# Kernel tuning notes

Measured on AMD Instinct MI355X. Metric: run time of the kernel, lower is better.

## Reference

```python
import jax, jax.numpy as jnp
import numpy as np

B, S, D = 4, 2048, 256
H = 8
KD = D  # keras MHA key_dim = input_shape[-1] -> per-head dim equals D
EPS = 1e-5


def layer_norm(x, gamma, beta):
    mu = jnp.mean(x, axis=-1, keepdims=True)
    var = jnp.var(x, axis=-1, keepdims=True)
    return (x - mu) * jax.lax.rsqrt(var + EPS) * gamma + beta


def setup_inputs() -> dict:
    key = jax.random.key(0)
    ks = jax.random.split(key, 12)
    scale = 1.0 / np.sqrt(D)
    inp = {
        "input_query": jax.random.normal(ks[0], (B, S, D), jnp.float32),
        "key": jax.random.normal(ks[1], (B, S, D), jnp.float32),
        "value": jax.random.normal(ks[2], (B, S, D), jnp.float32),
        # LayerNorm params (3 separate norms)
        "gq": jnp.ones((D,), jnp.float32), "bq_ln": jnp.zeros((D,), jnp.float32),
        "gk": jnp.ones((D,), jnp.float32), "bk_ln": jnp.zeros((D,), jnp.float32),
        "gv": jnp.ones((D,), jnp.float32), "bv_ln": jnp.zeros((D,), jnp.float32),
        # MHA projection weights: [D, H, KD] for q/k/v, [H, KD, D] for output
        "Wq": jax.random.normal(ks[3], (D, H, KD), jnp.float32) * scale,
        "bq": jnp.zeros((H, KD), jnp.float32),
        "Wk": jax.random.normal(ks[4], (D, H, KD), jnp.float32) * scale,
        "bk": jnp.zeros((H, KD), jnp.float32),
        "Wv": jax.random.normal(ks[5], (D, H, KD), jnp.float32) * scale,
        "bv": jnp.zeros((H, KD), jnp.float32),
        "Wo": jax.random.normal(ks[6], (H, KD, D), jnp.float32) * scale,
        "bo": jnp.zeros((D,), jnp.float32),
    }
    return inp


def reference(input_query, key, value, gq, bq_ln, gk, bk_ln, gv, bv_ln,
              Wq, bq, Wk, bk, Wv, bv, Wo, bo):
    # pre-LN on each stream
    q_in = layer_norm(input_query, gq, bq_ln)
    k_in = layer_norm(key, gk, bk_ln)
    v_in = layer_norm(value, gv, bv_ln)

    # projections -> [B, S, H, KD]
    q = jnp.einsum('bsd,dhk->bshk', q_in, Wq) + bq
    k = jnp.einsum('bsd,dhk->bshk', k_in, Wk) + bk
    v = jnp.einsum('bsd,dhk->bshk', v_in, Wv) + bv

    # scaled dot-product attention (keras scales query by 1/sqrt(key_dim))
    q = q * (1.0 / np.sqrt(KD)).astype(np.float32)
    scores = jnp.einsum('bqhk,bshk->bhqs', q, k)  # [B, H, Sq, Sk]
    probs = jax.nn.softmax(scores, axis=-1)
    # dropout = 0.0 (inference)
    attn = jnp.einsum('bhqs,bshk->bqhk', probs, v)
    out = jnp.einsum('bqhk,hkd->bqd', attn, Wo) + bo

    return input_query + out
```

## Files before the change

### kernel.cpp

```cpp
#include <hip/hip_runtime.h>

using bf16x8 = __attribute__((ext_vector_type(8))) __bf16;
using f32x4  = __attribute__((ext_vector_type(4))) float;
using f32x16 = __attribute__((ext_vector_type(16))) float;
using uint2v = __attribute__((ext_vector_type(2))) unsigned;
typedef unsigned short u16;
typedef const __attribute__((address_space(1))) void* gas_p;
typedef __attribute__((address_space(3))) void* las_p;

#define LOG2E 1.4426950408889634f

__device__ __forceinline__ u16 f2bf(float f) {
  union { float f; unsigned u; } v; v.f = f;
  unsigned r = v.u + 0x7fffu + ((v.u >> 16) & 1u);
  return (u16)(r >> 16);
}

__device__ __forceinline__ unsigned pkbf(float a, float b) {
  unsigned r;
  asm("v_cvt_pk_bf16_f32 %0, %1, %2" : "=v"(r) : "v"(a), "v"(b));
  return r;
}

__device__ __forceinline__ float exp2v(float x) {
  float r;
  asm("v_exp_f32 %0, %1" : "=v"(r) : "v"(x));
  return r;
}

__device__ __forceinline__ unsigned pk_fp8x4(float a, float b, float c, float d) {
  int w = __builtin_amdgcn_cvt_pk_fp8_f32(a, b, 0, false);
  w = __builtin_amdgcn_cvt_pk_fp8_f32(c, d, w, true);
  return (unsigned)w;
}

__device__ __forceinline__ uint2v swap32(unsigned a, unsigned b) {
  return __builtin_amdgcn_permlane32_swap(a, b, false, false);
}

__device__ __forceinline__ void gload16(const void* g, void* l) {
  __builtin_amdgcn_global_load_lds((gas_p)g, (las_p)l, 16, 0, 0);
}

#define MFMA(a, b, c)   __builtin_amdgcn_mfma_f32_16x16x32_bf16((a), (b), (c), 0, 0, 0)
#define MFMA32(a, b, c) __builtin_amdgcn_mfma_f32_32x32x16_bf16((a), (b), (c), 0, 0, 0)
#define MFMA8(a, b, c)  __builtin_amdgcn_mfma_f32_32x32x16_fp8_fp8((a), (b), (c), 0, 0, 0)

__global__ __launch_bounds__(256) void transpose_conv(
    const float* __restrict__ Wq, const float* __restrict__ Wk,
    const float* __restrict__ Wv, const float* __restrict__ Wo,
    u16* __restrict__ wqt, u16* __restrict__ wkt,
    u16* __restrict__ wvt, u16* __restrict__ wot)
{
  int z = blockIdx.y;
  const float* src = (z == 0) ? Wq : (z == 1) ? Wk : (z == 2) ? Wv : Wo;
  u16* dst = (z == 0) ? wqt : (z == 1) ? wkt : (z == 2) ? wvt : wot;
  int C = (z < 3) ? 2048 : 256;
  int R = (z < 3) ? 256 : 2048;
  int TC = C >> 5;
  int tc = blockIdx.x % TC, tr = blockIdx.x / TC;
  __shared__ float tile[32][33];
  int j = threadIdx.x & 31, i0 = threadIdx.x >> 5;
#pragma unroll
  for (int p = 0; p < 4; p++)
    tile[i0 + p * 8][j] = src[(tr * 32 + i0 + p * 8) * C + tc * 32 + j];
  __syncthreads();
#pragma unroll
  for (int p = 0; p < 4; p++)
    dst[(tc * 32 + i0 + p * 8) * R + tr * 32 + j] = f2bf(tile[j][i0 + p * 8]);
}

__global__ __launch_bounds__(256) void ln3_kernel(
    const float* __restrict__ xq, const float* __restrict__ xk, const float* __restrict__ xv,
    const float* __restrict__ gq, const float* __restrict__ bq,
    const float* __restrict__ gk, const float* __restrict__ bk,
    const float* __restrict__ gv, const float* __restrict__ bv,
    u16* __restrict__ oq, u16* __restrict__ ok, u16* __restrict__ ov)
{
  int z = blockIdx.y;
  const float* x = (z == 0) ? xq : (z == 1) ? xk : xv;
  const float* g = (z == 0) ? gq : (z == 1) ? gk : gv;
  const float* be = (z == 0) ? bq : (z == 1) ? bk : bv;
  u16* o = (z == 0) ? oq : (z == 1) ? ok : ov;
  int w = threadIdx.x >> 6, l = threadIdx.x & 63;
  int row = blockIdx.x * 4 + w;
  float4 x4 = *(const float4*)(x + row * 256 + l * 4);
  float s = x4.x + x4.y + x4.z + x4.w;
  float sq = x4.x * x4.x + x4.y * x4.y + x4.z * x4.z + x4.w * x4.w;
#pragma unroll
  for (int mm = 1; mm < 64; mm <<= 1) { s += __shfl_xor(s, mm); sq += __shfl_xor(sq, mm); }
  float mu = s * (1.f / 256.f);
  float var = sq * (1.f / 256.f) - mu * mu;
  float rs = rsqrtf(var + 1e-5f);
  float4 g4 = *(const float4*)(g + l * 4);
  float4 b4 = *(const float4*)(be + l * 4);
  ushort4 o4;
  o4.x = f2bf((x4.x - mu) * rs * g4.x + b4.x);
  o4.y = f2bf((x4.y - mu) * rs * g4.y + b4.y);
  o4.z = f2bf((x4.z - mu) * rs * g4.z + b4.z);
  o4.w = f2bf((x4.w - mu) * rs * g4.w + b4.w);
  *(ushort4*)(o + row * 256 + l * 4) = o4;
}

__global__ __launch_bounds__(256) void proj_gemm(
    const u16* __restrict__ qn, const u16* __restrict__ kn, const u16* __restrict__ vn,
    const u16* __restrict__ wqt, const u16* __restrict__ wkt, const u16* __restrict__ wvt,
    const float* __restrict__ bq, const float* __restrict__ bk, const float* __restrict__ bv,
    u16* __restrict__ qo, u16* __restrict__ ko, unsigned char* __restrict__ vo)
{
  __shared__ u16 As[128 * 64];
  __shared__ u16 Bs[128 * 64];
  int z = blockIdx.z;
  const u16* A  = (z == 0) ? qn : (z == 1) ? kn : vn;
  const u16* Bt = (z == 0) ? wqt : (z == 1) ? wkt : wvt;
  const float* bias = (z == 0) ? bq : (z == 1) ? bk : bv;
  float scale = (z == 0) ? 0.0625f * LOG2E : 1.0f;

  int i0 = blockIdx.x * 128, n0 = blockIdx.y * 128;
  int tid = threadIdx.x, w = tid >> 6, l = tid & 63;
  int wr = w >> 1, wc = w & 1, l15 = l & 15, qv = l >> 4;

  f32x4 acc[4][4] = {};

  for (int k0 = 0; k0 < 256; k0 += 64) {
    __syncthreads();
#pragma unroll
    for (int j = 0; j < 4; j++) {
      int c = (w * 4 + j) * 64 + l;
      int row = c >> 3, co = (c & 7) * 8;
      gload16(A + (i0 + row) * 256 + k0 + co, (char*)As + (w * 4 + j) * 1024);
      gload16(Bt + (n0 + row) * 256 + k0 + co, (char*)Bs + (w * 4 + j) * 1024);
    }
    __syncthreads();
#pragma unroll
    for (int kk = 0; kk < 2; kk++) {
      bf16x8 a[4], bfr[4];
#pragma unroll
      for (int m = 0; m < 4; m++)
        a[m] = *(const bf16x8*)(As + (wr * 64 + m * 16 + l15) * 64 + kk * 32 + qv * 8);
#pragma unroll
      for (int n = 0; n < 4; n++)
        bfr[n] = *(const bf16x8*)(Bs + (wc * 64 + n * 16 + l15) * 64 + kk * 32 + qv * 8);
#pragma unroll
      for (int m = 0; m < 4; m++)
#pragma unroll
        for (int n = 0; n < 4; n++) acc[m][n] = MFMA(a[m], bfr[n], acc[m][n]);
    }
  }

  if (z == 2) {
#pragma unroll
    for (int n = 0; n < 4; n++) {
      int col = n0 + wc * 64 + n * 16 + l15;
      float bc = bias[col];
      int hd = col >> 8, kd = col & 255;
#pragma unroll
      for (int m = 0; m < 4; m++) {
        int row0 = i0 + wr * 64 + m * 16 + qv * 4;
        int bb = row0 >> 11, ss = row0 & 2047;
        unsigned wv = pk_fp8x4(acc[m][n][0] + bc, acc[m][n][1] + bc,
                               acc[m][n][2] + bc, acc[m][n][3] + bc);
        int pos = (ss & ~63) | (((ss >> 3) & 3) << 4) | (((ss >> 5) & 1) << 3) | (ss & 7);
        *(unsigned*)(vo + ((size_t)(bb * 8 + hd) * 256 + kd) * 2048 + pos) = wv;
      }
    }
  } else {
    u16* Co = (z == 0) ? qo : ko;
#pragma unroll
    for (int n = 0; n < 4; n++) {
      int col = n0 + wc * 64 + n * 16 + l15;
      float bc = bias[col];
      int hd = col >> 8, kd = col & 255;
#pragma unroll
      for (int m = 0; m < 4; m++) {
#pragma unroll
        for (int r = 0; r < 4; r++) {
          int row = i0 + wr * 64 + m * 16 + qv * 4 + r;
          int bb = row >> 11, ss = row & 2047;
          Co[((bb * 8 + hd) * 2048 + ss) * 256 + kd] = f2bf((acc[m][n][r] + bc) * scale);
        }
      }
    }
  }
}

__global__ __launch_bounds__(512, 2) void flash_attn(
    const u16* __restrict__ q, const u16* __restrict__ k,
    const unsigned char* __restrict__ vt, u16* __restrict__ o)
{
  __shared__ char lds[98304];
  int f = blockIdx.x;
  int qt = f >> 5;
  int bh = (f & 7) | (((f >> 3) & 3) << 3);
  int b = bh >> 3, hh = bh & 7;
  int tid = threadIdx.x, w = tid >> 6, l = tid & 63;
  int l31 = l & 31, h = l >> 5;

  const u16* Q = q + (size_t)(bh * 2048 + qt * 256 + w * 32) * 256;
  const u16* K = k + (size_t)bh * 2048 * 256;
  const unsigned char* V = vt + (size_t)bh * 256 * 2048;

  bf16x8 qf[16];
#pragma unroll
  for (int dt = 0; dt < 16; dt++)
    qf[dt] = *(const bf16x8*)(Q + l31 * 256 + dt * 16 + h * 8);

  f32x16 oacc[8] = {};
  float m_ = -1e30f, lsum = 0.f;

  auto stage = [&](int t, char* base) {
#pragma unroll
    for (int j = 0; j < 4; j++) {
      int c = w * 4 + j;
      int off = c * 1024 + l * 16;
      int r = off >> 9, ps = l & 31;
      gload16(K + (size_t)(t * 64 + r) * 256 + ((ps ^ (r & 31)) << 3), base + off);
    }
#pragma unroll
    for (int j = 0; j < 2; j++) {
      int c = w * 2 + j;
      int off = c * 1024 + l * 16;
      int r = off >> 8, pg = (off >> 4) & 15;
      int g = pg ^ (r & 15);
      int d = r + 64 * (g >> 2), sc = g & 3;
      gload16(V + (size_t)d * 2048 + t * 64 + sc * 16, base + 32768 + off);
    }
  };

  stage(0, lds);
  __syncthreads();

  for (int t = 0; t < 32; t++) {
    char* cur = lds + (size_t)(t & 1) * 49152;
    char* nxt = lds + (size_t)((t + 1) & 1) * 49152;
    if (t + 1 < 32) stage(t + 1, nxt);

    f32x16 p0 = {}, p1 = {};
    __builtin_amdgcn_s_setprio(1);
#pragma unroll
    for (int dt = 0; dt < 16; dt++) {
      int sl = ((dt * 2 + h) ^ l31) << 4;
      bf16x8 kf0 = *(const bf16x8*)(cur + l31 * 512 + sl);
      bf16x8 kf1 = *(const bf16x8*)(cur + (32 + l31) * 512 + sl);
      p0 = MFMA32(kf0, qf[dt], p0);
      p1 = MFMA32(kf1, qf[dt], p1);
    }
    __builtin_amdgcn_s_setprio(0);

    float n0 = fmaxf(fmaxf(p0[0], p0[1]), fmaxf(p0[2], p0[3]));
    float n1 = fmaxf(fmaxf(p0[4], p0[5]), fmaxf(p0[6], p0[7]));
    float n2 = fmaxf(fmaxf(p0[8], p0[9]), fmaxf(p0[10], p0[11]));
    float n3 = fmaxf(fmaxf(p0[12], p0[13]), fmaxf(p0[14], p0[15]));
    float n4 = fmaxf(fmaxf(p1[0], p1[1]), fmaxf(p1[2], p1[3]));
    float n5 = fmaxf(fmaxf(p1[4], p1[5]), fmaxf(p1[6], p1[7]));
    float n6 = fmaxf(fmaxf(p1[8], p1[9]), fmaxf(p1[10], p1[11]));
    float n7 = fmaxf(fmaxf(p1[12], p1[13]), fmaxf(p1[14], p1[15]));
    float mt = fmaxf(fmaxf(fmaxf(n0, n1), fmaxf(n2, n3)),
                     fmaxf(fmaxf(n4, n5), fmaxf(n6, n7)));
    {
      uint2v mr = swap32(__builtin_bit_cast(unsigned, mt), __builtin_bit_cast(unsigned, mt));
      mt = fmaxf(__builtin_bit_cast(float, mr.x), __builtin_bit_cast(float, mr.y));
    }
    if (__any(mt > m_ + 7.0f)) {
      float mn = fmaxf(m_, mt);
      float fsc = exp2v(m_ - mn);
      lsum *= fsc;
#pragma unroll
      for (int dt = 0; dt < 8; dt++)
#pragma unroll
        for (int i = 0; i < 16; i++) oacc[dt][i] *= fsc;
      m_ = mn;
    }
#pragma unroll
    for (int i = 0; i < 16; i++) { p0[i] = exp2v(p0[i] - m_); lsum += p0[i]; }
#pragma unroll
    for (int i = 0; i < 16; i++) { p1[i] = exp2v(p1[i] - m_); lsum += p1[i]; }

    unsigned pwf0[4], pwf1[4];
#pragma unroll
    for (int j = 0; j < 4; j++) {
      pwf0[j] = pk_fp8x4(p0[4 * j], p0[4 * j + 1], p0[4 * j + 2], p0[4 * j + 3]);
      pwf1[j] = pk_fp8x4(p1[4 * j], p1[4 * j + 1], p1[4 * j + 2], p1[4 * j + 3]);
    }

#pragma unroll
    for (int k2 = 0; k2 < 2; k2++) {
      uint2v f0 = swap32(pwf0[k2 * 2], pwf0[k2 * 2 + 1]);
      uint2v f1 = swap32(pwf1[k2 * 2], pwf1[k2 * 2 + 1]);
      long long pA = (long long)(((unsigned long long)f0.y << 32) | f0.x);
      long long pB = (long long)(((unsigned long long)f1.y << 32) | f1.x);
      __builtin_amdgcn_s_setprio(1);
#pragma unroll
      for (int dt = 0; dt < 8; dt++) {
        int r = (dt & 1) * 32 + l31;
        int g = (dt >> 1) * 4 + k2 * 2 + h;
        const uint4 vv = *(const uint4*)(cur + 32768 + r * 256 + ((g ^ (r & 15)) << 4));
        long long vA = (long long)(((unsigned long long)vv.y << 32) | vv.x);
        long long vB = (long long)(((unsigned long long)vv.w << 32) | vv.z);
        oacc[dt] = MFMA8(vA, pA, oacc[dt]);
        oacc[dt] = MFMA8(vB, pB, oacc[dt]);
      }
      __builtin_amdgcn_s_setprio(0);
    }

    asm volatile("s_waitcnt vmcnt(0)" ::: "memory");
    __syncthreads();
  }

  __syncthreads();
  float lsc;
  {
    uint2v lr = swap32(__builtin_bit_cast(unsigned, lsum), __builtin_bit_cast(unsigned, lsum));
    lsc = __builtin_bit_cast(float, lr.x) + __builtin_bit_cast(float, lr.y);
  }
  float inv = 1.0f / lsc;
  char* wbase = (char*)lds + w * 8192;
  int qr15 = l31 & 15;
#pragma unroll
  for (int ph = 0; ph < 2; ph++) {
    if ((l31 >> 4) == ph) {
#pragma unroll
      for (int dt = 0; dt < 8; dt++) {
#pragma unroll
        for (int rg = 0; rg < 4; rg++) {
          uint2 uu;
          uu.x = pkbf(oacc[dt][rg * 4 + 0] * inv, oacc[dt][rg * 4 + 1] * inv);
          uu.y = pkbf(oacc[dt][rg * 4 + 2] * inv, oacc[dt][rg * 4 + 3] * inv);
          *(uint2*)(wbase + qr15 * 512 + ((dt * 64 + rg * 16) ^ (qr15 << 4)) + h * 8) = uu;
        }
      }
    }
    asm volatile("s_waitcnt lgkmcnt(0)" ::: "memory");
    __builtin_amdgcn_sched_barrier(0);
#pragma unroll
    for (int c = 0; c < 8; c++) {
      int qr = c * 2 + h;
      uint4 vv = *(const uint4*)(wbase + qr * 512 + ((l31 ^ qr) << 4));
      int s = qt * 256 + w * 32 + ph * 16 + qr;
      *(uint4*)((char*)o + (size_t)(b * 2048 + s) * 4096 + hh * 512 + l31 * 16) = vv;
    }
    asm volatile("s_waitcnt lgkmcnt(0)" ::: "memory");
  }
}

__global__ __launch_bounds__(256) void out_gemm(
    const u16* __restrict__ A, const u16* __restrict__ Bt,
    const float* __restrict__ bo, const float* __restrict__ resid,
    float* __restrict__ out)
{
  __shared__ u16 As[128 * 64];
  __shared__ u16 Bs[64 * 64];
  int i0 = blockIdx.x * 128, n0 = blockIdx.y * 64;
  int tid = threadIdx.x, w = tid >> 6, l = tid & 63, l15 = l & 15, qv = l >> 4;

  f32x4 acc[2][4] = {};

  for (int k0 = 0; k0 < 2048; k0 += 64) {
    __syncthreads();
#pragma unroll
    for (int j = 0; j < 4; j++) {
      int c = (w * 4 + j) * 64 + l;
      int row = c >> 3, co = (c & 7) * 8;
      gload16(A + (i0 + row) * 2048 + k0 + co, (char*)As + (w * 4 + j) * 1024);
    }
#pragma unroll
    for (int j = 0; j < 2; j++) {
      int c = (w * 2 + j) * 64 + l;
      int row = c >> 3, co = (c & 7) * 8;
      gload16(Bt + (n0 + row) * 2048 + k0 + co, (char*)Bs + (w * 2 + j) * 1024);
    }
    __syncthreads();
#pragma unroll
    for (int kk = 0; kk < 2; kk++) {
      bf16x8 a[2], bfr[4];
#pragma unroll
      for (int m = 0; m < 2; m++)
        a[m] = *(const bf16x8*)(As + (w * 32 + m * 16 + l15) * 64 + kk * 32 + qv * 8);
#pragma unroll
      for (int n = 0; n < 4; n++)
        bfr[n] = *(const bf16x8*)(Bs + (n * 16 + l15) * 64 + kk * 32 + qv * 8);
#pragma unroll
      for (int m = 0; m < 2; m++)
#pragma unroll
        for (int n = 0; n < 4; n++) acc[m][n] = MFMA(a[m], bfr[n], acc[m][n]);
    }
  }

#pragma unroll
  for (int n = 0; n < 4; n++) {
    int col = n0 + n * 16 + l15;
    float bc = bo[col];
#pragma unroll
    for (int m = 0; m < 2; m++)
#pragma unroll
      for (int r = 0; r < 4; r++) {
        int row = i0 + w * 32 + m * 16 + qv * 4 + r;
        out[row * 256 + col] = acc[m][n][r] + bc + resid[row * 256 + col];
      }
  }
}

extern "C" void kernel_launch(void* const* d_in, const int* in_sizes, int n_in,
                              void* d_out, int out_size, void* d_ws, size_t ws_size,
                              hipStream_t stream)
{
  const float* inq  = (const float*)d_in[0];
  const float* key  = (const float*)d_in[1];
  const float* val  = (const float*)d_in[2];
  const float* gq   = (const float*)d_in[3];
  const float* bqln = (const float*)d_in[4];
  const float* gk   = (const float*)d_in[5];
  const float* bkln = (const float*)d_in[6];
  const float* gv   = (const float*)d_in[7];
  const float* bvln = (const float*)d_in[8];
  const float* Wq   = (const float*)d_in[9];
  const float* bq   = (const float*)d_in[10];
  const float* Wk   = (const float*)d_in[11];
  const float* bk   = (const float*)d_in[12];
  const float* Wv   = (const float*)d_in[13];
  const float* bv   = (const float*)d_in[14];
  const float* Wo   = (const float*)d_in[15];
  const float* bo   = (const float*)d_in[16];

  char* ws = (char*)d_ws;
  const size_t MB = 1ull << 20;
  u16* wqt = (u16*)(ws + 0 * MB);
  u16* wkt = (u16*)(ws + 1 * MB);
  u16* wvt = (u16*)(ws + 2 * MB);
  u16* wot = (u16*)(ws + 3 * MB);
  u16* qn  = (u16*)(ws + 4 * MB);
  u16* kn  = (u16*)(ws + 8 * MB);
  u16* vn  = (u16*)(ws + 12 * MB);
  u16* qws = (u16*)(ws + 16 * MB);
  u16* kws = (u16*)(ws + 48 * MB);
  u16* attn = (u16*)(ws + 80 * MB);
  unsigned char* vtw = (unsigned char*)(ws + 112 * MB);

  transpose_conv<<<dim3(512, 4), 256, 0, stream>>>(Wq, Wk, Wv, Wo, wqt, wkt, wvt, wot);
  ln3_kernel<<<dim3(2048, 3), 256, 0, stream>>>(inq, key, val, gq, bqln, gk, bkln, gv, bvln,
                                                qn, kn, vn);
  proj_gemm<<<dim3(64, 16, 3), 256, 0, stream>>>(qn, kn, vn, wqt, wkt, wvt, bq, bk, bv,
                                                 qws, kws, vtw);
  flash_attn<<<256, 512, 0, stream>>>(qws, kws, vtw, attn);
  out_gemm<<<dim3(64, 4), 256, 0, stream>>>(attn, wot, bo, inq, (float*)d_out);
}
```

Measured before the change: 251.5 us.

## Software-pipeline attention loop: defer PV of previous tile behind next QK

Restructures the flash-attention main loop so the P·V MFMAs for tile t-1 are issued right after the QK MFMAs for tile t, overlapping the softmax exp/max work with matrix-core work. K and V staging are split into separate double-buffered LDS regions, with K prefetched two tiles ahead and V one ahead. The per-iteration barrier moves to the end, just before the next loads are issued. The exp-sum reduction is split into four partial accumulators to shorten the dependency chain. This adds register pressure from carrying the packed probabilities between iterations, and the output rescale is now applied after the deferred PV has already accumulated into oacc.

```diff
diff --git a/kernel.cpp b/kernel.cpp
--- a/kernel.cpp
+++ b/kernel.cpp
@@ -207,8 +207,10 @@
 
   f32x16 oacc[8] = {};
   float m_ = -1e30f, lsum = 0.f;
-
-  auto stage = [&](int t, char* base) {
+  unsigned pwp0[4], pwp1[4];
+
+  auto stageK = [&](int t, int slot) {
+    char* base = lds + (size_t)slot * 32768;
 #pragma unroll
     for (int j = 0; j < 4; j++) {
       int c = w * 4 + j;
@@ -216,6 +218,9 @@
       int r = off >> 9, ps = l & 31;
       gload16(K + (size_t)(t * 64 + r) * 256 + ((ps ^ (r & 31)) << 3), base + off);
     }
+  };
+  auto stageV = [&](int t, int slot) {
+    char* base = lds + 65536 + (size_t)slot * 16384;
 #pragma unroll
     for (int j = 0; j < 2; j++) {
       int c = w * 2 + j;
@@ -223,29 +228,51 @@
       int r = off >> 8, pg = (off >> 4) & 15;
       int g = pg ^ (r & 15);
       int d = r + 64 * (g >> 2), sc = g & 3;
-      gload16(V + (size_t)d * 2048 + t * 64 + sc * 16, base + 32768 + off);
+      gload16(V + (size_t)d * 2048 + t * 64 + sc * 16, base + off);
     }
   };
 
-  stage(0, lds);
+  auto pv_prev = [&](const char* vb) {
+#pragma unroll
+    for (int k2 = 0; k2 < 2; k2++) {
+      uint2v f0 = swap32(pwp0[k2 * 2], pwp0[k2 * 2 + 1]);
+      uint2v f1 = swap32(pwp1[k2 * 2], pwp1[k2 * 2 + 1]);
+      long long pA = (long long)(((unsigned long long)f0.y << 32) | f0.x);
+      long long pB = (long long)(((unsigned long long)f1.y << 32) | f1.x);
+      __builtin_amdgcn_s_setprio(1);
+#pragma unroll
+      for (int dt = 0; dt < 8; dt++) {
+        int r = (dt & 1) * 32 + l31;
+        int g = (dt >> 1) * 4 + k2 * 2 + h;
+        const uint4 vv = *(const uint4*)(vb + r * 256 + ((g ^ (r & 15)) << 4));
+        long long vA = (long long)(((unsigned long long)vv.y << 32) | vv.x);
+        long long vB = (long long)(((unsigned long long)vv.w << 32) | vv.z);
+        oacc[dt] = MFMA8(vA, pA, oacc[dt]);
+        oacc[dt] = MFMA8(vB, pB, oacc[dt]);
+      }
+      __builtin_amdgcn_s_setprio(0);
+    }
+  };
+
+  stageK(0, 0); stageK(1, 1); stageV(0, 0);
   __syncthreads();
 
   for (int t = 0; t < 32; t++) {
-    char* cur = lds + (size_t)(t & 1) * 49152;
-    char* nxt = lds + (size_t)((t + 1) & 1) * 49152;
-    if (t + 1 < 32) stage(t + 1, nxt);
+    const char* kb = lds + (size_t)(t & 1) * 32768;
 
     f32x16 p0 = {}, p1 = {};
     __builtin_amdgcn_s_setprio(1);
 #pragma unroll
     for (int dt = 0; dt < 16; dt++) {
       int sl = ((dt * 2 + h) ^ l31) << 4;
-      bf16x8 kf0 = *(const bf16x8*)(cur + l31 * 512 + sl);
-      bf16x8 kf1 = *(const bf16x8*)(cur + (32 + l31) * 512 + sl);
+      bf16x8 kf0 = *(const bf16x8*)(kb + l31 * 512 + sl);
+      bf16x8 kf1 = *(const bf16x8*)(kb + (32 + l31) * 512 + sl);
       p0 = MFMA32(kf0, qf[dt], p0);
       p1 = MFMA32(kf1, qf[dt], p1);
     }
     __builtin_amdgcn_s_setprio(0);
+
+    if (t > 0) pv_prev(lds + 65536 + (size_t)((t - 1) & 1) * 16384);
 
     float n0 = fmaxf(fmaxf(p0[0], p0[1]), fmaxf(p0[2], p0[3]));
     float n1 = fmaxf(fmaxf(p0[4], p0[5]), fmaxf(p0[6], p0[7]));
@@ -261,20 +288,30 @@
       uint2v mr = swap32(__builtin_bit_cast(unsigned, mt), __builtin_bit_cast(unsigned, mt));
       mt = fmaxf(__builtin_bit_cast(float, mr.x), __builtin_bit_cast(float, mr.y));
     }
-    if (__any(mt > m_ + 7.0f)) {
+    bool resc = __any(mt > m_ + 7.0f);
+    float fsc = 1.0f;
+    if (resc) {
       float mn = fmaxf(m_, mt);
-      float fsc = exp2v(m_ - mn);
+      fsc = exp2v(m_ - mn);
       lsum *= fsc;
-#pragma unroll
-      for (int dt = 0; dt < 8; dt++)
-#pragma unroll
-        for (int i = 0; i < 16; i++) oacc[dt][i] *= fsc;
       m_ = mn;
     }
-#pragma unroll
-    for (int i = 0; i < 16; i++) { p0[i] = exp2v(p0[i] - m_); lsum += p0[i]; }
-#pragma unroll
-    for (int i = 0; i < 16; i++) { p1[i] = exp2v(p1[i] - m_); lsum += p1[i]; }
+    float s0 = 0.f, s1 = 0.f, s2 = 0.f, s3 = 0.f;
+#pragma unroll
+    for (int i = 0; i < 16; i += 4) {
+      p0[i] = exp2v(p0[i] - m_);         s0 += p0[i];
+      p0[i + 1] = exp2v(p0[i + 1] - m_); s1 += p0[i + 1];
+      p0[i + 2] = exp2v(p0[i + 2] - m_); s2 += p0[i + 2];
+      p0[i + 3] = exp2v(p0[i + 3] - m_); s3 += p0[i + 3];
+    }
+#pragma unroll
+    for (int i = 0; i < 16; i += 4) {
+      p1[i] = exp2v(p1[i] - m_);         s0 += p1[i];
+      p1[i + 1] = exp2v(p1[i + 1] - m_); s1 += p1[i + 1];
+      p1[i + 2] = exp2v(p1[i + 2] - m_); s2 += p1[i + 2];
+      p1[i + 3] = exp2v(p1[i + 3] - m_); s3 += p1[i + 3];
+    }
+    lsum += (s0 + s1) + (s2 + s3);
 
     unsigned pwf0[4], pwf1[4];
 #pragma unroll
@@ -283,29 +320,23 @@
       pwf1[j] = pk_fp8x4(p1[4 * j], p1[4 * j + 1], p1[4 * j + 2], p1[4 * j + 3]);
     }
 
-#pragma unroll
-    for (int k2 = 0; k2 < 2; k2++) {
-      uint2v f0 = swap32(pwf0[k2 * 2], pwf0[k2 * 2 + 1]);
-      uint2v f1 = swap32(pwf1[k2 * 2], pwf1[k2 * 2 + 1]);
-      long long pA = (long long)(((unsigned long long)f0.y << 32) | f0.x);
-      long long pB = (long long)(((unsigned long long)f1.y << 32) | f1.x);
-      __builtin_amdgcn_s_setprio(1);
-#pragma unroll
-      for (int dt = 0; dt < 8; dt++) {
-        int r = (dt & 1) * 32 + l31;
-        int g = (dt >> 1) * 4 + k2 * 2 + h;
-        const uint4 vv = *(const uint4*)(cur + 32768 + r * 256 + ((g ^ (r & 15)) << 4));
-        long long vA = (long long)(((unsigned long long)vv.y << 32) | vv.x);
-        long long vB = (long long)(((unsigned long long)vv.w << 32) | vv.z);
-        oacc[dt] = MFMA8(vA, pA, oacc[dt]);
-        oacc[dt] = MFMA8(vB, pB, oacc[dt]);
-      }
-      __builtin_amdgcn_s_setprio(0);
-    }
-
-    asm volatile("s_waitcnt vmcnt(0)" ::: "memory");
-    __syncthreads();
-  }
+    if (resc) {
+#pragma unroll
+      for (int dt = 0; dt < 8; dt++)
+#pragma unroll
+        for (int i = 0; i < 16; i++) oacc[dt][i] *= fsc;
+    }
+
+#pragma unroll
+    for (int j = 0; j < 4; j++) { pwp0[j] = pwf0[j]; pwp1[j] = pwf1[j]; }
+
+    asm volatile("s_waitcnt vmcnt(0) lgkmcnt(0)" ::: "memory");
+    __builtin_amdgcn_s_barrier();
+    if (t + 2 < 32) stageK(t + 2, t & 1);
+    if (t + 1 < 32) stageV(t + 1, (t + 1) & 1);
+  }
+
+  pv_prev(lds + 65536 + (size_t)(31 & 1) * 16384);
 
   __syncthreads();
   float lsc;
```

After: 263.3 us. 4.7% more time.
